# Optimization experiments

Measured on AMD Instinct MI355X. Metric: run time of the kernel, lower is better.

Reference implementation:

```python
import jax, jax.numpy as jnp
import numpy as np

D_MODEL = 1024
NUM_HEADS = 16
D_K = D_MODEL // NUM_HEADS  # 64
THETA = 10000.0
MAX_SEQ_LEN = 2048


def _trunc_normal(key, shape, std):
    # approximate trunc_normal_(mean=0, std, a=-3*std, b=3*std)
    u = jax.random.truncated_normal(key, -3.0, 3.0, shape, dtype=jnp.float32)
    return u * std


def setup_inputs() -> dict:
    key = jax.random.key(0)
    ks = jax.random.split(key, 5)
    x = jax.random.normal(ks[0], (2, 2048, D_MODEL), dtype=jnp.float32)
    token_positions = jnp.arange(2048, dtype=jnp.int64 if jax.config.jax_enable_x64 else jnp.int32)
    sigma = 2.0 / (D_MODEL + D_MODEL)
    Wq = _trunc_normal(ks[1], (D_MODEL, D_MODEL), sigma)
    Wk = _trunc_normal(ks[2], (D_MODEL, D_MODEL), sigma)
    Wv = _trunc_normal(ks[3], (D_MODEL, D_MODEL), sigma)
    Wo = _trunc_normal(ks[4], (D_MODEL, D_MODEL), sigma)
    return {"in_features": x, "Wq": Wq, "Wk": Wk, "Wv": Wv, "Wo": Wo,
            "token_positions": token_positions}


def _rope(x, cos_phi, sin_phi):
    # x: (..., seq, d_k); cos/sin: (seq, d_k//2)
    x_even = x[..., 0::2]
    x_odd = x[..., 1::2]
    y_even = x_even * cos_phi - x_odd * sin_phi
    y_odd = x_even * sin_phi + x_odd * cos_phi
    # interleave back
    y = jnp.stack([y_even, y_odd], axis=-1)
    return y.reshape(x.shape)


def reference(in_features, Wq, Wk, Wv, Wo, token_positions):
    b, s, d = in_features.shape
    h, dk = NUM_HEADS, D_K
    # projections: weight is (d_out, d_in)
    q = jnp.einsum('bsd,ed->bse', in_features, Wq)
    k = jnp.einsum('bsd,ed->bse', in_features, Wk)
    v = jnp.einsum('bsd,ed->bse', in_features, Wv)
    # split heads: (b, h, s, dk)
    q = q.reshape(b, s, h, dk).transpose(0, 2, 1, 3)
    k = k.reshape(b, s, h, dk).transpose(0, 2, 1, 3)
    v = v.reshape(b, s, h, dk).transpose(0, 2, 1, 3)
    # RoPE tables
    inv_freq = 1.0 / (THETA ** (jnp.arange(0, dk, 2, dtype=jnp.float32) / dk))
    phi = token_positions.astype(jnp.float32)[:, None] * inv_freq[None, :]  # (s, dk/2)
    cos_phi, sin_phi = jnp.cos(phi), jnp.sin(phi)
    q = _rope(q, cos_phi, sin_phi)
    k = _rope(k, cos_phi, sin_phi)
    # causal mask
    mask = jnp.tril(jnp.ones((s, s), dtype=bool))
    scores = jnp.einsum('bhqd,bhkd->bhqk', q, k) / jnp.sqrt(jnp.float32(dk))
    scores = jnp.where(mask, scores, -jnp.inf)
    attn = jax.nn.softmax(scores, axis=-1)
    out = jnp.einsum('bhqk,bhkd->bhqd', attn, v)
    out = out.transpose(0, 2, 1, 3).reshape(b, s, d)
    return jnp.einsum('bsd,ed->bse', out, Wo)
```

## Files before the change

kernel.cpp:

```cpp
#include <hip/hip_runtime.h>
#include <hip/hip_bf16.h>
#include <math.h>

#define S_  2048
#define DM_ 1024

typedef unsigned short u16;
typedef __attribute__((ext_vector_type(8))) short short8;
typedef __attribute__((ext_vector_type(4))) float f32x4;

__device__ __forceinline__ u16 f2bf(float f) {
  unsigned u = __float_as_uint(f);
  u += 0x7fffu + ((u >> 16) & 1u);
  return (u16)(u >> 16);
}
__device__ __forceinline__ float bf2f(u16 h) {
  return __uint_as_float((unsigned)h << 16);
}
__device__ __forceinline__ unsigned pack_bf2(float a, float b) {
  union { __hip_bfloat162 h2; unsigned u; } cv;
  cv.h2 = __float22bfloat162_rn(float2{a, b});
  return cv.u;
}
__device__ __forceinline__ void cp16(const void* g, void* l) {
  __builtin_amdgcn_global_load_lds(
      (const __attribute__((address_space(1))) unsigned*)(uintptr_t)g,
      (__attribute__((address_space(3))) unsigned*)(unsigned)(uintptr_t)l, 16, 0, 0);
}

struct CastArgs { const float* src[5]; u16* dst[5]; int n[5]; };

__global__ __launch_bounds__(256) void cast_kernel(CastArgs a) {
  const int z = blockIdx.y;
  const int i = (blockIdx.x * 256 + threadIdx.x) * 8;
  if (i >= a.n[z]) return;
  const float4* s = (const float4*)(a.src[z] + i);
  float4 v0 = s[0], v1 = s[1];
  short8 r;
  r[0] = (short)f2bf(v0.x); r[1] = (short)f2bf(v0.y);
  r[2] = (short)f2bf(v0.z); r[3] = (short)f2bf(v0.w);
  r[4] = (short)f2bf(v1.x); r[5] = (short)f2bf(v1.y);
  r[6] = (short)f2bf(v1.z); r[7] = (short)f2bf(v1.w);
  *(short8*)(a.dst[z] + i) = r;
}

struct GemmArgs { const u16* A; const u16* W[3]; void* out[3]; const int* tp; int modes; };

template<int GXL>
__global__ __launch_bounds__(256, 2) void gemm_mfma(GemmArgs g) {
  constexpr int BM = 128, BN = 64;
  constexpr int ABYTES = BM * 64 * 2;
  constexpr int SLOT = ABYTES + BN * 64 * 2;
  __shared__ __align__(16) char lds[3 * SLOT];

  const int tid = threadIdx.x, lane = tid & 63, w = tid >> 6;
  const int wm = w >> 1, wn = w & 1;
  const int t = lane & 15, u = lane >> 4;
  const int l3 = lane >> 3, l7 = lane & 7;
  const int z = blockIdx.z;

  const int nwg = (int)gridDim.y << GXL;
  const int flat = (int)blockIdx.x + ((int)blockIdx.y << GXL);
  const int swz = (flat & 7) * (nwg >> 3) + (flat >> 3);
  const int m0 = (swz >> GXL) * BM;
  const int n0 = (swz & ((1 << GXL) - 1)) * BN;

  const u16* __restrict__ A = g.A;
  const u16* __restrict__ W = g.W[z];

  const int axor = l7 << 4;
  const int ksw = (l7 ^ l3) * 8;
  const u16* Ab = A + (size_t)(m0 + l3) * 1024 + ksw;
  const u16* Wb = W + (size_t)(n0 + l3) * 1024 + ksw;

  auto stg = [&](char* sb, int kt) {
    #pragma unroll
    for (int r = 0; r < 4; r++)
      cp16(Ab + (size_t)(w * 4 + r) * 8192 + kt * 64, sb + (w * 4 + r) * 1024);
    #pragma unroll
    for (int r = 0; r < 2; r++)
      cp16(Wb + (size_t)(w * 2 + r) * 8192 + kt * 64, sb + ABYTES + (w * 2 + r) * 1024);
  };

  const f32x4 fz = {0.f, 0.f, 0.f, 0.f};
  f32x4 acc[4][2];
  #pragma unroll
  for (int i = 0; i < 4; i++) { acc[i][0] = fz; acc[i][1] = fz; }

  stg(lds, 0);
  stg(lds + SLOT, 1);
  asm volatile("s_waitcnt vmcnt(6)" ::: "memory");
  __builtin_amdgcn_s_barrier();

  int rs_ = 0, ss_ = 2;
  for (int kt = 0; kt < 16; kt++) {
    const char* cs = lds + rs_ * SLOT;
    if (kt + 2 < 16) stg(lds + ss_ * SLOT, kt + 2);

    short8 af[2][4], bfr[2][2];
    #pragma unroll
    for (int ks = 0; ks < 2; ks++) {
      const int co = (ks * 64 + u * 16) ^ axor;
      const char* ap = cs + (wm * 64 + t) * 128 + co;
      const char* bp = cs + ABYTES + (wn * 32 + t) * 128 + co;
      #pragma unroll
      for (int mf = 0; mf < 4; mf++) af[ks][mf] = *(const short8*)(ap + mf * 2048);
      #pragma unroll
      for (int nf = 0; nf < 2; nf++) bfr[ks][nf] = *(const short8*)(bp + nf * 2048);
    }
    asm volatile("s_waitcnt lgkmcnt(0)" ::: "memory");
    __builtin_amdgcn_sched_barrier(0);
    __builtin_amdgcn_s_setprio(1);
    #pragma unroll
    for (int ks = 0; ks < 2; ks++)
      #pragma unroll
      for (int mf = 0; mf < 4; mf++)
        #pragma unroll
        for (int nf = 0; nf < 2; nf++)
          acc[mf][nf] = __builtin_amdgcn_mfma_f32_16x16x32_bf16(af[ks][mf], bfr[ks][nf], acc[mf][nf], 0, 0, 0);
    __builtin_amdgcn_s_setprio(0);

    if (kt + 2 < 16)      { asm volatile("s_waitcnt vmcnt(6)" ::: "memory"); }
    else if (kt + 1 < 16) { asm volatile("s_waitcnt vmcnt(0)" ::: "memory"); }
    __builtin_amdgcn_s_barrier();
    rs_ = (rs_ == 2) ? 0 : rs_ + 1;
    ss_ = (ss_ == 2) ? 0 : ss_ + 1;
  }

  const int mode = (g.modes >> (2 * z)) & 3;
  const int rbase = m0 + wm * 64 + u * 4;
  const int cbase = n0 + wn * 32 + t;
  if (mode == 0) {
    u16* O = (u16*)g.out[z];
    #pragma unroll
    for (int mt = 0; mt < 4; mt++)
      #pragma unroll
      for (int nt = 0; nt < 2; nt++)
        #pragma unroll
        for (int r = 0; r < 4; r++)
          O[(size_t)(rbase + mt * 16 + r) * 1024 + cbase + nt * 16] = f2bf(acc[mt][nt][r]);
  } else if (mode == 1) {
    u16* O = (u16*)g.out[z];
    #pragma unroll
    for (int mt = 0; mt < 4; mt++)
      #pragma unroll
      for (int nt = 0; nt < 2; nt++) {
        int gr = rbase + mt * 16;
        int b = gr >> 11, s0 = gr & (S_ - 1);
        int gc = cbase + nt * 16;
        int h = gc >> 6, d = gc & 63;
        ushort4 v;
        v.x = f2bf(acc[mt][nt][0]); v.y = f2bf(acc[mt][nt][1]);
        v.z = f2bf(acc[mt][nt][2]); v.w = f2bf(acc[mt][nt][3]);
        *(ushort4*)&O[(size_t)((b * 16 + h) * 64 + d) * 2048 + s0] = v;
      }
  } else if (mode == 2) {
    float* O = (float*)g.out[z];
    #pragma unroll
    for (int mt = 0; mt < 4; mt++)
      #pragma unroll
      for (int nt = 0; nt < 2; nt++)
        #pragma unroll
        for (int r = 0; r < 4; r++)
          O[(size_t)(rbase + mt * 16 + r) * 1024 + cbase + nt * 16] = acc[mt][nt][r];
  } else {
    u16* O = (u16*)g.out[z];
    const float osc = (z == 0) ? 0.18033688011112042f : 1.0f;
    const float sgn = (cbase & 1) ? 1.0f : -1.0f;
    #pragma unroll
    for (int mt = 0; mt < 4; mt++)
      #pragma unroll
      for (int r = 0; r < 4; r++) {
        const int gr = rbase + mt * 16 + r;
        const float pos = (float)g.tp[gr & (S_ - 1)];
        #pragma unroll
        for (int nt = 0; nt < 2; nt++) {
          const int d = (cbase + nt * 16) & 63;
          const float x = acc[mt][nt][r];
          const float p = __shfl_xor(x, 1, 64);
          const float inv = exp2f(-(float)(d & ~1) * 0.20762050593046439f);
          float sn, cs;
          sincosf(pos * inv, &sn, &cs);
          O[(size_t)gr * 1024 + cbase + nt * 16] = f2bf((x * cs + p * sgn * sn) * osc);
        }
      }
  }
}

__global__ __launch_bounds__(512, 4) void attn_mfma(const u16* __restrict__ qb, const u16* __restrict__ kb,
                                                    const u16* __restrict__ vt, u16* __restrict__ ab) {
  __shared__ __align__(16) u16 Qs[2][4096];
  __shared__ __align__(16) u16 Ks[2][4096];
  __shared__ __align__(16) u16 Vs[2][4096];

  const int tid = threadIdx.x, lane = tid & 63, w = tid >> 6;
  const int v = w & 3, g = w >> 2;
  const int t = lane & 15, u = lane >> 4;
  const int bh = blockIdx.y, b = bh >> 4, h = bh & 15;
  const int i = blockIdx.x;
  const int qa = 31 - i;
  const int qbt = i;
  const int nk = 32 - i;
  const size_t qkb = (size_t)b * S_ * 1024 + h * 64;
  const size_t vtb = (size_t)bh * 64 * 2048;

  {
    const int qtile = g ? qbt : qa;
    cp16(qb + qkb + (size_t)(qtile * 64 + lane) * 1024 + v * 8,       (char*)Qs[g] + v * 1024);
    cp16(qb + qkb + (size_t)(qtile * 64 + lane) * 1024 + (v + 4) * 8, (char*)Qs[g] + 4096 + v * 1024);
  }
  cp16(kb + qkb + (size_t)lane * 1024 + w * 8, (char*)Ks[0] + w * 1024);
  cp16(vt + vtb + (size_t)lane * 2048 + w * 8, (char*)Vs[0] + w * 1024);
  __syncthreads();

  short8 aqA[2], aqP[2];
  #pragma unroll
  for (int ks = 0; ks < 2; ks++) {
    aqA[ks] = *(const short8*)((const char*)Qs[0] + (ks * 4 + u) * 1024 + (v * 16 + t) * 16);
    short8 bq = *(const short8*)((const char*)Qs[1] + (ks * 4 + u) * 1024 + (v * 16 + t) * 16);
    aqP[ks] = g ? bq : aqA[ks];
  }

  const f32x4 fzero = {0.f, 0.f, 0.f, 0.f};
  f32x4 oPrim[4], oSec[4];
  #pragma unroll
  for (int ct = 0; ct < 4; ct++) { oPrim[ct] = fzero; oSec[ct] = fzero; }
  float rsumP = 0.f, rsumS = 0.f;

  const int qprim = g ? qbt : qa;
  const int qrowP = qprim * 64 + v * 16 + t;
  const int qrowA = qa * 64 + v * 16 + t;

  for (int kt = 0; kt < nk; kt++) {
    const int cur = kt & 1, nxt = cur ^ 1;
    if (kt + 1 < nk) {
      cp16(kb + qkb + (size_t)((kt + 1) * 64 + lane) * 1024 + w * 8, (char*)Ks[nxt] + w * 1024);
      cp16(vt + vtb + (size_t)lane * 2048 + (kt + 1) * 64 + w * 8,   (char*)Vs[nxt] + w * 1024);
    }

    if (kt <= qbt) {
      f32x4 st[4] = {fzero, fzero, fzero, fzero};
      __builtin_amdgcn_s_setprio(1);
      #pragma unroll
      for (int ks = 0; ks < 2; ks++)
        #pragma unroll
        for (int ct = 0; ct < 4; ct++) {
          short8 kf = *(const short8*)((const char*)Ks[cur] + (ks * 4 + u) * 1024 + (ct * 16 + t) * 16);
          st[ct] = __builtin_amdgcn_mfma_f32_16x16x32_bf16(kf, aqP[ks], st[ct], 0, 0, 0);
        }
      __builtin_amdgcn_s_setprio(0);

      unsigned pb2[4][2];
      if (kt == qprim) {
        #pragma unroll
        for (int ct = 0; ct < 4; ct++) {
          float p[4];
          #pragma unroll
          for (int r = 0; r < 4; r++) {
            int key = kt * 64 + ct * 16 + 4 * u + r;
            float pv = exp2f(st[ct][r]);
            p[r] = (key > qrowP) ? 0.f : pv;
          }
          rsumP += (p[0] + p[1]) + (p[2] + p[3]);
          pb2[ct][0] = pack_bf2(p[0], p[1]);
          pb2[ct][1] = pack_bf2(p[2], p[3]);
        }
      } else {
        #pragma unroll
        for (int ct = 0; ct < 4; ct++) {
          float p[4];
          #pragma unroll
          for (int r = 0; r < 4; r++) p[r] = exp2f(st[ct][r]);
          rsumP += (p[0] + p[1]) + (p[2] + p[3]);
          pb2[ct][0] = pack_bf2(p[0], p[1]);
          pb2[ct][1] = pack_bf2(p[2], p[3]);
        }
      }

      #pragma unroll
      for (int ks = 0; ks < 2; ks++) {
        union { short8 s8; int i4[4]; } pf;
        #pragma unroll
        for (int jj = 0; jj < 4; jj++) {
          int src = 32 * (u & 1) + 16 * (jj >> 1) + t;
          int v0 = __shfl((int)pb2[ks * 2][jj & 1], src, 64);
          int v1 = __shfl((int)pb2[ks * 2 + 1][jj & 1], src, 64);
          pf.i4[jj] = (u >> 1) ? v1 : v0;
        }
        __builtin_amdgcn_s_setprio(1);
        #pragma unroll
        for (int ct = 0; ct < 4; ct++) {
          short8 vf = *(const short8*)((const char*)Vs[cur] + (ks * 4 + u) * 1024 + (ct * 16 + t) * 16);
          oPrim[ct] = __builtin_amdgcn_mfma_f32_16x16x32_bf16(vf, pf.s8, oPrim[ct], 0, 0, 0);
        }
        __builtin_amdgcn_s_setprio(0);
      }
    } else {
      f32x4 st2[2] = {fzero, fzero};
      __builtin_amdgcn_s_setprio(1);
      #pragma unroll
      for (int ks = 0; ks < 2; ks++)
        #pragma unroll
        for (int c = 0; c < 2; c++) {
          short8 kf = *(const short8*)((const char*)Ks[cur] + (ks * 4 + u) * 1024 + ((2 * g + c) * 16 + t) * 16);
          st2[c] = __builtin_amdgcn_mfma_f32_16x16x32_bf16(kf, aqA[ks], st2[c], 0, 0, 0);
        }
      __builtin_amdgcn_s_setprio(0);

      unsigned ph[2][2];
      float rs = 0.f;
      if (kt == qa) {
        #pragma unroll
        for (int c = 0; c < 2; c++) {
          float p[4];
          #pragma unroll
          for (int r = 0; r < 4; r++) {
            int key = kt * 64 + (2 * g + c) * 16 + 4 * u + r;
            float pv = exp2f(st2[c][r]);
            p[r] = (key > qrowA) ? 0.f : pv;
          }
          rs += (p[0] + p[1]) + (p[2] + p[3]);
          ph[c][0] = pack_bf2(p[0], p[1]);
          ph[c][1] = pack_bf2(p[2], p[3]);
        }
      } else {
        #pragma unroll
        for (int c = 0; c < 2; c++) {
          float p[4];
          #pragma unroll
          for (int r = 0; r < 4; r++) p[r] = exp2f(st2[c][r]);
          rs += (p[0] + p[1]) + (p[2] + p[3]);
          ph[c][0] = pack_bf2(p[0], p[1]);
          ph[c][1] = pack_bf2(p[2], p[3]);
        }
      }

      union { short8 s8; int i4[4]; } pf;
      #pragma unroll
      for (int jj = 0; jj < 4; jj++) {
        int src = 32 * (u & 1) + 16 * (jj >> 1) + t;
        int v0 = __shfl((int)ph[0][jj & 1], src, 64);
        int v1 = __shfl((int)ph[1][jj & 1], src, 64);
        pf.i4[jj] = (u >> 1) ? v1 : v0;
      }
      if (g) {
        rsumS += rs;
        __builtin_amdgcn_s_setprio(1);
        #pragma unroll
        for (int ct = 0; ct < 4; ct++) {
          short8 vf = *(const short8*)((const char*)Vs[cur] + (4 + u) * 1024 + (ct * 16 + t) * 16);
          oSec[ct] = __builtin_amdgcn_mfma_f32_16x16x32_bf16(vf, pf.s8, oSec[ct], 0, 0, 0);
        }
        __builtin_amdgcn_s_setprio(0);
      } else {
        rsumP += rs;
        __builtin_amdgcn_s_setprio(1);
        #pragma unroll
        for (int ct = 0; ct < 4; ct++) {
          short8 vf = *(const short8*)((const char*)Vs[cur] + u * 1024 + (ct * 16 + t) * 16);
          oPrim[ct] = __builtin_amdgcn_mfma_f32_16x16x32_bf16(vf, pf.s8, oPrim[ct], 0, 0, 0);
        }
        __builtin_amdgcn_s_setprio(0);
      }
    }
    __syncthreads();
  }

  float* dmpO = (float*)Ks;
  float* dmpR = (float*)Vs;
  if (g) {
    #pragma unroll
    for (int ct = 0; ct < 4; ct++)
      *(f32x4*)&dmpO[(size_t)(v * 64 + lane) * 16 + ct * 4] = oSec[ct];
    dmpR[v * 64 + lane] = rsumS;
    float rs = rsumP;
    rs += __shfl_xor(rs, 16, 64);
    rs += __shfl_xor(rs, 32, 64);
    const float inv = 1.0f / rs;
    #pragma unroll
    for (int ct = 0; ct < 4; ct++) {
      ushort4 vv;
      vv.x = f2bf(oPrim[ct][0] * inv); vv.y = f2bf(oPrim[ct][1] * inv);
      vv.z = f2bf(oPrim[ct][2] * inv); vv.w = f2bf(oPrim[ct][3] * inv);
      *(ushort4*)&ab[((size_t)b * S_ + qrowP) * 1024 + h * 64 + ct * 16 + 4 * u] = vv;
    }
  }
  __syncthreads();
  if (!g) {
    #pragma unroll
    for (int ct = 0; ct < 4; ct++) {
      f32x4 add = *(const f32x4*)&dmpO[(size_t)(v * 64 + lane) * 16 + ct * 4];
      oPrim[ct] += add;
    }
    float rs = rsumP + dmpR[v * 64 + lane];
    rs += __shfl_xor(rs, 16, 64);
    rs += __shfl_xor(rs, 32, 64);
    const float inv = 1.0f / rs;
    #pragma unroll
    for (int ct = 0; ct < 4; ct++) {
      ushort4 vv;
      vv.x = f2bf(oPrim[ct][0] * inv); vv.y = f2bf(oPrim[ct][1] * inv);
      vv.z = f2bf(oPrim[ct][2] * inv); vv.w = f2bf(oPrim[ct][3] * inv);
      *(ushort4*)&ab[((size_t)b * S_ + qrowA) * 1024 + h * 64 + ct * 16 + 4 * u] = vv;
    }
  }
}

extern "C" void kernel_launch(void* const* d_in, const int* in_sizes, int n_in,
                              void* d_out, int out_size, void* d_ws, size_t ws_size,
                              hipStream_t stream) {
  const float* x  = (const float*)d_in[0];
  const float* Wq = (const float*)d_in[1];
  const float* Wk = (const float*)d_in[2];
  const float* Wv = (const float*)d_in[3];
  const float* Wo = (const float*)d_in[4];
  const int*   tp = (const int*)d_in[5];
  float* out = (float*)d_out;

  char* ws = (char*)d_ws;
  u16* xb  = (u16*)(ws);
  u16* wqb = (u16*)(ws + (8 << 20));
  u16* wkb = (u16*)(ws + (10 << 20));
  u16* wvb = (u16*)(ws + (12 << 20));
  u16* wob = (u16*)(ws + (14 << 20));
  u16* qbuf = (u16*)(ws + (16 << 20));
  u16* kbuf = (u16*)(ws + (24 << 20));
  u16* vtb  = (u16*)(ws + (32 << 20));
  u16* abuf = (u16*)(ws + (40 << 20));

  CastArgs ca;
  ca.src[0] = x;  ca.dst[0] = xb;  ca.n[0] = 2 * S_ * DM_;
  ca.src[1] = Wq; ca.dst[1] = wqb; ca.n[1] = DM_ * DM_;
  ca.src[2] = Wk; ca.dst[2] = wkb; ca.n[2] = DM_ * DM_;
  ca.src[3] = Wv; ca.dst[3] = wvb; ca.n[3] = DM_ * DM_;
  ca.src[4] = Wo; ca.dst[4] = wob; ca.n[4] = DM_ * DM_;
  cast_kernel<<<dim3(2048, 5), 256, 0, stream>>>(ca);

  GemmArgs gq;
  gq.A = xb;
  gq.W[0] = wqb; gq.W[1] = wkb; gq.W[2] = wvb;
  gq.out[0] = qbuf; gq.out[1] = kbuf; gq.out[2] = vtb;
  gq.tp = tp;
  gq.modes = 3 | (3 << 2) | (1 << 4);
  gemm_mfma<4><<<dim3(16, 32, 3), 256, 0, stream>>>(gq);

  attn_mfma<<<dim3(16, 32), 512, 0, stream>>>(qbuf, kbuf, vtb, abuf);

  GemmArgs go;
  go.A = abuf;
  go.W[0] = wob; go.W[1] = wob; go.W[2] = wob;
  go.out[0] = out; go.out[1] = out; go.out[2] = out;
  go.tp = tp;
  go.modes = 2;
  gemm_mfma<4><<<dim3(16, 32, 1), 256, 0, stream>>>(go);
}
```

Before: 186.6 us.

## Fuse Q/K/V projections per block with register-resident A and swizzle attention LDS

The QKV projection now runs as one launch in which each block computes all three outputs for its tile, so each A tile is read once and reused across the three weight matrices. A fragments are loaded straight from global memory into registers with a double-buffered prefetch, and only the weight tiles are staged through LDS. The attention kernel gains an XOR swizzle on LDS rows for Q, K and V to reduce bank conflicts. In exchange the GEMM holds three times as many accumulators, which raises register pressure and may limit occupancy, and the direct global A loads lose LDS staging.

```diff
diff --git a/kernel.cpp b/kernel.cpp
--- a/kernel.cpp
+++ b/kernel.cpp
@@ -46,144 +46,151 @@
 
 struct GemmArgs { const u16* A; const u16* W[3]; void* out[3]; const int* tp; int modes; };
 
-template<int GXL>
+template<int NZ>
 __global__ __launch_bounds__(256, 2) void gemm_mfma(GemmArgs g) {
-  constexpr int BM = 128, BN = 64;
-  constexpr int ABYTES = BM * 64 * 2;
-  constexpr int SLOT = ABYTES + BN * 64 * 2;
+  constexpr int SLOT = NZ * 8192;
   __shared__ __align__(16) char lds[3 * SLOT];
 
   const int tid = threadIdx.x, lane = tid & 63, w = tid >> 6;
   const int wm = w >> 1, wn = w & 1;
   const int t = lane & 15, u = lane >> 4;
   const int l3 = lane >> 3, l7 = lane & 7;
-  const int z = blockIdx.z;
-
-  const int nwg = (int)gridDim.y << GXL;
-  const int flat = (int)blockIdx.x + ((int)blockIdx.y << GXL);
-  const int swz = (flat & 7) * (nwg >> 3) + (flat >> 3);
-  const int m0 = (swz >> GXL) * BM;
-  const int n0 = (swz & ((1 << GXL) - 1)) * BN;
-
-  const u16* __restrict__ A = g.A;
-  const u16* __restrict__ W = g.W[z];
+
+  const int flat = (int)blockIdx.x + ((int)blockIdx.y << 4);
+  const int swz = (flat & 7) * 64 + (flat >> 3);
+  const int m0 = (swz >> 4) * 128;
+  const int n0 = (swz & 15) * 64;
 
   const int axor = l7 << 4;
   const int ksw = (l7 ^ l3) * 8;
-  const u16* Ab = A + (size_t)(m0 + l3) * 1024 + ksw;
-  const u16* Wb = W + (size_t)(n0 + l3) * 1024 + ksw;
-
-  auto stg = [&](char* sb, int kt) {
-    #pragma unroll
-    for (int r = 0; r < 4; r++)
-      cp16(Ab + (size_t)(w * 4 + r) * 8192 + kt * 64, sb + (w * 4 + r) * 1024);
-    #pragma unroll
-    for (int r = 0; r < 2; r++)
-      cp16(Wb + (size_t)(w * 2 + r) * 8192 + kt * 64, sb + ABYTES + (w * 2 + r) * 1024);
+  const u16* Wb[NZ];
+  #pragma unroll
+  for (int z = 0; z < NZ; z++) Wb[z] = g.W[z] + (size_t)(n0 + l3) * 1024 + ksw;
+  const u16* Arow = g.A + (size_t)(m0 + wm * 64 + t) * 1024 + u * 8;
+
+  auto stgB = [&](char* sb, int kt) {
+    #pragma unroll
+    for (int z = 0; z < NZ; z++)
+      #pragma unroll
+      for (int r = 0; r < 2; r++)
+        cp16(Wb[z] + (size_t)(w * 2 + r) * 8192 + kt * 64, sb + z * 8192 + (w * 2 + r) * 1024);
   };
+  auto loadA = [&](short8 (&af)[2][4], int kt) {
+    #pragma unroll
+    for (int ks = 0; ks < 2; ks++)
+      #pragma unroll
+      for (int mf = 0; mf < 4; mf++)
+        af[ks][mf] = *(const short8*)(Arow + (size_t)mf * 16384 + kt * 64 + ks * 32);
+  };
 
   const f32x4 fz = {0.f, 0.f, 0.f, 0.f};
-  f32x4 acc[4][2];
+  f32x4 acc[NZ][4][2];
   #pragma unroll
-  for (int i = 0; i < 4; i++) { acc[i][0] = fz; acc[i][1] = fz; }
-
-  stg(lds, 0);
-  stg(lds + SLOT, 1);
-  asm volatile("s_waitcnt vmcnt(6)" ::: "memory");
+  for (int z = 0; z < NZ; z++)
+    #pragma unroll
+    for (int i = 0; i < 4; i++) { acc[z][i][0] = fz; acc[z][i][1] = fz; }
+
+  short8 af0[2][4], af1[2][4];
+  loadA(af0, 0);
+  stgB(lds, 0);
+  stgB(lds + SLOT, 1);
+  if constexpr (NZ == 3) { asm volatile("s_waitcnt vmcnt(6)" ::: "memory"); }
+  else                   { asm volatile("s_waitcnt vmcnt(2)" ::: "memory"); }
   __builtin_amdgcn_s_barrier();
 
   int rs_ = 0, ss_ = 2;
-  for (int kt = 0; kt < 16; kt++) {
+  auto tile = [&](int kt, short8 (&afU)[2][4], short8 (&afL)[2][4]) {
     const char* cs = lds + rs_ * SLOT;
-    if (kt + 2 < 16) stg(lds + ss_ * SLOT, kt + 2);
-
-    short8 af[2][4], bfr[2][2];
-    #pragma unroll
-    for (int ks = 0; ks < 2; ks++) {
-      const int co = (ks * 64 + u * 16) ^ axor;
-      const char* ap = cs + (wm * 64 + t) * 128 + co;
-      const char* bp = cs + ABYTES + (wn * 32 + t) * 128 + co;
-      #pragma unroll
-      for (int mf = 0; mf < 4; mf++) af[ks][mf] = *(const short8*)(ap + mf * 2048);
-      #pragma unroll
-      for (int nf = 0; nf < 2; nf++) bfr[ks][nf] = *(const short8*)(bp + nf * 2048);
-    }
+    if (kt + 1 < 16) loadA(afL, kt + 1);
+    if (kt + 2 < 16) stgB(lds + ss_ * SLOT, kt + 2);
+
+    short8 bfr[NZ][2][2];
+    #pragma unroll
+    for (int z = 0; z < NZ; z++)
+      #pragma unroll
+      for (int ks = 0; ks < 2; ks++) {
+        const int co = (ks * 64 + u * 16) ^ axor;
+        const char* bp = cs + z * 8192 + (wn * 32 + t) * 128 + co;
+        bfr[z][ks][0] = *(const short8*)(bp);
+        bfr[z][ks][1] = *(const short8*)(bp + 2048);
+      }
     asm volatile("s_waitcnt lgkmcnt(0)" ::: "memory");
     __builtin_amdgcn_sched_barrier(0);
     __builtin_amdgcn_s_setprio(1);
     #pragma unroll
     for (int ks = 0; ks < 2; ks++)
       #pragma unroll
-      for (int mf = 0; mf < 4; mf++)
-        #pragma unroll
-        for (int nf = 0; nf < 2; nf++)
-          acc[mf][nf] = __builtin_amdgcn_mfma_f32_16x16x32_bf16(af[ks][mf], bfr[ks][nf], acc[mf][nf], 0, 0, 0);
+      for (int z = 0; z < NZ; z++)
+        #pragma unroll
+        for (int mf = 0; mf < 4; mf++)
+          #pragma unroll
+          for (int nf = 0; nf < 2; nf++)
+            acc[z][mf][nf] = __builtin_amdgcn_mfma_f32_16x16x32_bf16(afU[ks][mf], bfr[z][ks][nf], acc[z][mf][nf], 0, 0, 0);
     __builtin_amdgcn_s_setprio(0);
 
-    if (kt + 2 < 16)      { asm volatile("s_waitcnt vmcnt(6)" ::: "memory"); }
-    else if (kt + 1 < 16) { asm volatile("s_waitcnt vmcnt(0)" ::: "memory"); }
+    if (kt + 2 < 16) {
+      if constexpr (NZ == 3) { asm volatile("s_waitcnt vmcnt(6)" ::: "memory"); }
+      else                   { asm volatile("s_waitcnt vmcnt(2)" ::: "memory"); }
+    } else if (kt + 1 < 16) {
+      asm volatile("s_waitcnt vmcnt(0)" ::: "memory");
+    }
     __builtin_amdgcn_s_barrier();
     rs_ = (rs_ == 2) ? 0 : rs_ + 1;
     ss_ = (ss_ == 2) ? 0 : ss_ + 1;
-  }
-
-  const int mode = (g.modes >> (2 * z)) & 3;
+  };
+  for (int k2 = 0; k2 < 16; k2 += 2) { tile(k2, af0, af1); tile(k2 + 1, af1, af0); }
+
   const int rbase = m0 + wm * 64 + u * 4;
   const int cbase = n0 + wn * 32 + t;
-  if (mode == 0) {
-    u16* O = (u16*)g.out[z];
-    #pragma unroll
-    for (int mt = 0; mt < 4; mt++)
-      #pragma unroll
-      for (int nt = 0; nt < 2; nt++)
-        #pragma unroll
-        for (int r = 0; r < 4; r++)
-          O[(size_t)(rbase + mt * 16 + r) * 1024 + cbase + nt * 16] = f2bf(acc[mt][nt][r]);
-  } else if (mode == 1) {
-    u16* O = (u16*)g.out[z];
-    #pragma unroll
-    for (int mt = 0; mt < 4; mt++)
-      #pragma unroll
-      for (int nt = 0; nt < 2; nt++) {
-        int gr = rbase + mt * 16;
-        int b = gr >> 11, s0 = gr & (S_ - 1);
-        int gc = cbase + nt * 16;
-        int h = gc >> 6, d = gc & 63;
-        ushort4 v;
-        v.x = f2bf(acc[mt][nt][0]); v.y = f2bf(acc[mt][nt][1]);
-        v.z = f2bf(acc[mt][nt][2]); v.w = f2bf(acc[mt][nt][3]);
-        *(ushort4*)&O[(size_t)((b * 16 + h) * 64 + d) * 2048 + s0] = v;
-      }
-  } else if (mode == 2) {
-    float* O = (float*)g.out[z];
-    #pragma unroll
-    for (int mt = 0; mt < 4; mt++)
-      #pragma unroll
-      for (int nt = 0; nt < 2; nt++)
-        #pragma unroll
-        for (int r = 0; r < 4; r++)
-          O[(size_t)(rbase + mt * 16 + r) * 1024 + cbase + nt * 16] = acc[mt][nt][r];
-  } else {
-    u16* O = (u16*)g.out[z];
-    const float osc = (z == 0) ? 0.18033688011112042f : 1.0f;
-    const float sgn = (cbase & 1) ? 1.0f : -1.0f;
-    #pragma unroll
-    for (int mt = 0; mt < 4; mt++)
-      #pragma unroll
-      for (int r = 0; r < 4; r++) {
-        const int gr = rbase + mt * 16 + r;
-        const float pos = (float)g.tp[gr & (S_ - 1)];
+  #pragma unroll
+  for (int z = 0; z < NZ; z++) {
+    const int mode = (g.modes >> (2 * z)) & 3;
+    if (mode == 1) {
+      u16* O = (u16*)g.out[z];
+      #pragma unroll
+      for (int mt = 0; mt < 4; mt++)
         #pragma unroll
         for (int nt = 0; nt < 2; nt++) {
-          const int d = (cbase + nt * 16) & 63;
-          const float x = acc[mt][nt][r];
-          const float p = __shfl_xor(x, 1, 64);
-          const float inv = exp2f(-(float)(d & ~1) * 0.20762050593046439f);
-          float sn, cs;
-          sincosf(pos * inv, &sn, &cs);
-          O[(size_t)gr * 1024 + cbase + nt * 16] = f2bf((x * cs + p * sgn * sn) * osc);
-        }
-      }
+          int gr = rbase + mt * 16;
+          int b = gr >> 11, s0 = gr & (S_ - 1);
+          int gc = cbase + nt * 16;
+          int h = gc >> 6, d = gc & 63;
+          ushort4 v;
+          v.x = f2bf(acc[z][mt][nt][0]); v.y = f2bf(acc[z][mt][nt][1]);
+          v.z = f2bf(acc[z][mt][nt][2]); v.w = f2bf(acc[z][mt][nt][3]);
+          *(ushort4*)&O[(size_t)((b * 16 + h) * 64 + d) * 2048 + s0] = v;
+        }
+    } else if (mode == 2) {
+      float* O = (float*)g.out[z];
+      #pragma unroll
+      for (int mt = 0; mt < 4; mt++)
+        #pragma unroll
+        for (int nt = 0; nt < 2; nt++)
+          #pragma unroll
+          for (int r = 0; r < 4; r++)
+            O[(size_t)(rbase + mt * 16 + r) * 1024 + cbase + nt * 16] = acc[z][mt][nt][r];
+    } else if (mode == 3) {
+      u16* O = (u16*)g.out[z];
+      const float osc = (z == 0) ? 0.18033688011112042f : 1.0f;
+      const float sgn = (cbase & 1) ? 1.0f : -1.0f;
+      #pragma unroll
+      for (int mt = 0; mt < 4; mt++)
+        #pragma unroll
+        for (int r = 0; r < 4; r++) {
+          const int gr = rbase + mt * 16 + r;
+          const float pos = (float)g.tp[gr & (S_ - 1)];
+          #pragma unroll
+          for (int nt = 0; nt < 2; nt++) {
+            const int d = (cbase + nt * 16) & 63;
+            const float x = acc[z][mt][nt][r];
+            const float p = __shfl_xor(x, 1, 64);
+            const float inv = exp2f(-(float)(d & ~1) * 0.20762050593046439f);
+            float sn, cs;
+            sincosf(pos * inv, &sn, &cs);
+            O[(size_t)gr * 1024 + cbase + nt * 16] = f2bf((x * cs + p * sgn * sn) * osc);
+          }
+        }
+    }
   }
 }
 
@@ -203,21 +210,27 @@
   const int nk = 32 - i;
   const size_t qkb = (size_t)b * S_ * 1024 + h * 64;
   const size_t vtb = (size_t)bh * 64 * 2048;
+  const int ux2 = u << 1;
 
   {
     const int qtile = g ? qbt : qa;
-    cp16(qb + qkb + (size_t)(qtile * 64 + lane) * 1024 + v * 8,       (char*)Qs[g] + v * 1024);
-    cp16(qb + qkb + (size_t)(qtile * 64 + lane) * 1024 + (v + 4) * 8, (char*)Qs[g] + 4096 + v * 1024);
-  }
-  cp16(kb + qkb + (size_t)lane * 1024 + w * 8, (char*)Ks[0] + w * 1024);
-  cp16(vt + vtb + (size_t)lane * 2048 + w * 8, (char*)Vs[0] + w * 1024);
+    const int lsw = lane ^ (v << 1);
+    cp16(qb + qkb + (size_t)(qtile * 64 + lsw) * 1024 + v * 8,       (char*)Qs[g] + v * 1024);
+    cp16(qb + qkb + (size_t)(qtile * 64 + lsw) * 1024 + (v + 4) * 8, (char*)Qs[g] + 4096 + v * 1024);
+  }
+  {
+    const int lsw = lane ^ ((w & 3) << 1);
+    cp16(kb + qkb + (size_t)lsw * 1024 + w * 8, (char*)Ks[0] + w * 1024);
+    cp16(vt + vtb + (size_t)lsw * 2048 + w * 8, (char*)Vs[0] + w * 1024);
+  }
   __syncthreads();
 
   short8 aqA[2], aqP[2];
   #pragma unroll
   for (int ks = 0; ks < 2; ks++) {
-    aqA[ks] = *(const short8*)((const char*)Qs[0] + (ks * 4 + u) * 1024 + (v * 16 + t) * 16);
-    short8 bq = *(const short8*)((const char*)Qs[1] + (ks * 4 + u) * 1024 + (v * 16 + t) * 16);
+    const int ro = ((v * 16 + t) ^ ux2) * 16;
+    aqA[ks] = *(const short8*)((const char*)Qs[0] + (ks * 4 + u) * 1024 + ro);
+    short8 bq = *(const short8*)((const char*)Qs[1] + (ks * 4 + u) * 1024 + ro);
     aqP[ks] = g ? bq : aqA[ks];
   }
 
@@ -234,8 +247,9 @@
   for (int kt = 0; kt < nk; kt++) {
     const int cur = kt & 1, nxt = cur ^ 1;
     if (kt + 1 < nk) {
-      cp16(kb + qkb + (size_t)((kt + 1) * 64 + lane) * 1024 + w * 8, (char*)Ks[nxt] + w * 1024);
-      cp16(vt + vtb + (size_t)lane * 2048 + (kt + 1) * 64 + w * 8,   (char*)Vs[nxt] + w * 1024);
+      const int lsw = lane ^ ((w & 3) << 1);
+      cp16(kb + qkb + (size_t)((kt + 1) * 64 + lsw) * 1024 + w * 8, (char*)Ks[nxt] + w * 1024);
+      cp16(vt + vtb + (size_t)lsw * 2048 + (kt + 1) * 64 + w * 8,   (char*)Vs[nxt] + w * 1024);
     }
 
     if (kt <= qbt) {
@@ -245,7 +259,7 @@
       for (int ks = 0; ks < 2; ks++)
         #pragma unroll
         for (int ct = 0; ct < 4; ct++) {
-          short8 kf = *(const short8*)((const char*)Ks[cur] + (ks * 4 + u) * 1024 + (ct * 16 + t) * 16);
+          short8 kf = *(const short8*)((const char*)Ks[cur] + (ks * 4 + u) * 1024 + ((ct * 16 + t) ^ ux2) * 16);
           st[ct] = __builtin_amdgcn_mfma_f32_16x16x32_bf16(kf, aqP[ks], st[ct], 0, 0, 0);
         }
       __builtin_amdgcn_s_setprio(0);
@@ -290,7 +304,7 @@
         __builtin_amdgcn_s_setprio(1);
         #pragma unroll
         for (int ct = 0; ct < 4; ct++) {
-          short8 vf = *(const short8*)((const char*)Vs[cur] + (ks * 4 + u) * 1024 + (ct * 16 + t) * 16);
+          short8 vf = *(const short8*)((const char*)Vs[cur] + (ks * 4 + u) * 1024 + ((ct * 16 + t) ^ ux2) * 16);
           oPrim[ct] = __builtin_amdgcn_mfma_f32_16x16x32_bf16(vf, pf.s8, oPrim[ct], 0, 0, 0);
         }
         __builtin_amdgcn_s_setprio(0);
@@ -302,7 +316,7 @@
       for (int ks = 0; ks < 2; ks++)
         #pragma unroll
         for (int c = 0; c < 2; c++) {
-          short8 kf = *(const short8*)((const char*)Ks[cur] + (ks * 4 + u) * 1024 + ((2 * g + c) * 16 + t) * 16);
+          short8 kf = *(const short8*)((const char*)Ks[cur] + (ks * 4 + u) * 1024 + (((2 * g + c) * 16 + t) ^ ux2) * 16);
           st2[c] = __builtin_amdgcn_mfma_f32_16x16x32_bf16(kf, aqA[ks], st2[c], 0, 0, 0);
         }
       __builtin_amdgcn_s_setprio(0);
@@ -348,7 +362,7 @@
         __builtin_amdgcn_s_setprio(1);
         #pragma unroll
         for (int ct = 0; ct < 4; ct++) {
-          short8 vf = *(const short8*)((const char*)Vs[cur] + (4 + u) * 1024 + (ct * 16 + t) * 16);
+          short8 vf = *(const short8*)((const char*)Vs[cur] + (4 + u) * 1024 + ((ct * 16 + t) ^ ux2) * 16);
           oSec[ct] = __builtin_amdgcn_mfma_f32_16x16x32_bf16(vf, pf.s8, oSec[ct], 0, 0, 0);
         }
         __builtin_amdgcn_s_setprio(0);
@@ -357,7 +371,7 @@
         __builtin_amdgcn_s_setprio(1);
         #pragma unroll
         for (int ct = 0; ct < 4; ct++) {
-          short8 vf = *(const short8*)((const char*)Vs[cur] + u * 1024 + (ct * 16 + t) * 16);
+          short8 vf = *(const short8*)((const char*)Vs[cur] + u * 1024 + ((ct * 16 + t) ^ ux2) * 16);
           oPrim[ct] = __builtin_amdgcn_mfma_f32_16x16x32_bf16(vf, pf.s8, oPrim[ct], 0, 0, 0);
         }
         __builtin_amdgcn_s_setprio(0);
@@ -442,7 +456,7 @@
   gq.out[0] = qbuf; gq.out[1] = kbuf; gq.out[2] = vtb;
   gq.tp = tp;
   gq.modes = 3 | (3 << 2) | (1 << 4);
-  gemm_mfma<4><<<dim3(16, 32, 3), 256, 0, stream>>>(gq);
+  gemm_mfma<3><<<dim3(16, 32), 256, 0, stream>>>(gq);
 
   attn_mfma<<<dim3(16, 32), 512, 0, stream>>>(qbuf, kbuf, vtb, abuf);
 
@@ -452,5 +466,5 @@
   go.out[0] = out; go.out[1] = out; go.out[2] = out;
   go.tp = tp;
   go.modes = 2;
-  gemm_mfma<4><<<dim3(16, 32, 1), 256, 0, stream>>>(go);
-}
+  gemm_mfma<1><<<dim3(16, 32), 256, 0, stream>>>(go);
+}
```

Result: slower. 245.6 us (+31.6%).
